# Performance work log

Hardware: AMD Instinct MI355X
Metric: run time of the kernel (lower is better)

## Reference

```python
import jax, jax.numpy as jnp
import numpy as np

HARDLIM_THRESH = 0.2


def setup_inputs() -> dict:
    key = jax.random.key(0)
    k_inp, k_w1, k_b1, k_w2, k_b2 = jax.random.split(key, 5)
    B, D, H, F = 16384, 4096, 2048, 512
    scale1 = 1.0 / np.sqrt(D)
    scale2 = 1.0 / np.sqrt(H)
    return {
        "inp": jax.random.normal(k_inp, (B, D), dtype=jnp.float32),
        "W1": jax.random.normal(k_w1, (H, D), dtype=jnp.float32) * scale1,
        "b1": jax.random.normal(k_b1, (H,), dtype=jnp.float32) * scale1,
        "W2": jax.random.normal(k_w2, (F, H), dtype=jnp.float32) * scale2,
        "b2": jax.random.normal(k_b2, (F,), dtype=jnp.float32) * scale2,
        "k": 8,
    }


def reference(inp, W1, b1, W2, b2, k):
    # Linear -> ReLU -> Linear
    h = jax.nn.relu(inp @ W1.T + b1)            # [B, H]
    logits = h @ W2.T + b2                      # [B, F]
    # 'hard' attention: sigmoid -> keep top-k (zero the rest) -> hardlim(0.2)
    s = jax.nn.sigmoid(logits)
    topk_vals, _ = jax.lax.top_k(s, k)          # [B, k]
    kth = topk_vals[:, -1:]                     # per-row k-th largest value
    gated = jnp.where(s >= kth, s, 0.0)         # GetTopK: zero non-top-k entries
    out = jnp.where(gated > HARDLIM_THRESH, 1.0, 0.0).astype(inp.dtype)
    return out
```

## Files before the change

kernel.cpp:

```cpp
#include <hip/hip_runtime.h>
#include <math.h>
#include <type_traits>


#define BM 128
#define BN 128
#define BK 16
#define BKF 32

#define TAU   1.0e-4f
#define L02F -1.3862943611198906f

typedef __attribute__((ext_vector_type(8))) short bf16x8;
typedef __attribute__((ext_vector_type(4))) float f32x4;

__device__ inline ushort bfhi(float f)   { return (ushort)(__float_as_uint(f) >> 16); }
__device__ inline float  bfhif(float f)  { return __uint_as_float(__float_as_uint(f) & 0xFFFF0000u); }

__global__ __launch_bounds__(256) void split_kernel(
    const float* __restrict__ src, ushort* __restrict__ hi,
    ushort* __restrict__ lo, size_t n4)
{
    size_t i = (size_t)blockIdx.x * 256 + threadIdx.x;
    size_t stride = (size_t)gridDim.x * 256;
    for (; i < n4; i += stride) {
        float4 v = ((const float4*)src)[i];
        ushort4 h, l;
        h.x = bfhi(v.x); l.x = bfhi(v.x - bfhif(v.x));
        h.y = bfhi(v.y); l.y = bfhi(v.y - bfhif(v.y));
        h.z = bfhi(v.z); l.z = bfhi(v.z - bfhif(v.z));
        h.w = bfhi(v.w); l.w = bfhi(v.w - bfhif(v.w));
        ((ushort4*)hi)[i] = h;
        ((ushort4*)lo)[i] = l;
    }
}

template<int A_PRESPLIT, int W_PRESPLIT, int OUT_MODE>
__global__ __launch_bounds__(256) void bgemm_split(
    const float*  __restrict__ A32,
    const ushort* __restrict__ Ahg, const ushort* __restrict__ Alg, int lda,
    const float*  __restrict__ W32,
    const ushort* __restrict__ Whg, const ushort* __restrict__ Wlg, int ldw,
    const float*  __restrict__ bias,
    ushort* __restrict__ Chi, ushort* __restrict__ Clo,
    float*  __restrict__ C32, int N, int K)
{
    __shared__ __align__(16) ushort Ah[BM * BKF];
    __shared__ __align__(16) ushort Al[BM * BKF];
    __shared__ __align__(16) ushort Bh[BN * BKF];
    __shared__ __align__(16) ushort Bl[BN * BKF];

    const int t    = threadIdx.x;
    const int lane = t & 63;
    const int wave = t >> 6;
    const int wr   = wave >> 1;
    const int wc   = wave & 1;
    const int l15  = lane & 15;
    const int l4   = lane >> 4;
    const size_t bm = blockIdx.x;
    const size_t bn = blockIdx.y;

    f32x4 acc[4][4];
    #pragma unroll
    for (int mi = 0; mi < 4; ++mi)
        #pragma unroll
        for (int ni = 0; ni < 4; ++ni)
            acc[mi][ni] = (f32x4){0.f, 0.f, 0.f, 0.f};

    for (int k0 = 0; k0 < K; k0 += BKF) {
        if (A_PRESPLIT) {
            #pragma unroll
            for (int i = 0; i < 2; ++i) {
                int c = t + i * 256;
                int row = c >> 2, q = c & 3;
                size_t g = (bm * BM + row) * (size_t)lda + k0 + q * 8;
                *(uint4*)&Ah[row * BKF + q * 8] = *(const uint4*)(Ahg + g);
                *(uint4*)&Al[row * BKF + q * 8] = *(const uint4*)(Alg + g);
            }
        } else {
            #pragma unroll
            for (int i = 0; i < 4; ++i) {
                int c = t + i * 256;
                int row = c >> 3, q = c & 7;
                float4 v = *(const float4*)(A32 + (bm * BM + row) * (size_t)lda + k0 + q * 4);
                ushort4 h, l;
                h.x = bfhi(v.x); l.x = bfhi(v.x - bfhif(v.x));
                h.y = bfhi(v.y); l.y = bfhi(v.y - bfhif(v.y));
                h.z = bfhi(v.z); l.z = bfhi(v.z - bfhif(v.z));
                h.w = bfhi(v.w); l.w = bfhi(v.w - bfhif(v.w));
                *(ushort4*)&Ah[row * BKF + q * 4] = h;
                *(ushort4*)&Al[row * BKF + q * 4] = l;
            }
        }
        if (W_PRESPLIT) {
            #pragma unroll
            for (int i = 0; i < 2; ++i) {
                int c = t + i * 256;
                int row = c >> 2, q = c & 3;
                size_t g = (bn * BN + row) * (size_t)ldw + k0 + q * 8;
                *(uint4*)&Bh[row * BKF + q * 8] = *(const uint4*)(Whg + g);
                *(uint4*)&Bl[row * BKF + q * 8] = *(const uint4*)(Wlg + g);
            }
        } else {
            #pragma unroll
            for (int i = 0; i < 4; ++i) {
                int c = t + i * 256;
                int row = c >> 3, q = c & 7;
                float4 v = *(const float4*)(W32 + (bn * BN + row) * (size_t)ldw + k0 + q * 4);
                ushort4 h, l;
                h.x = bfhi(v.x); l.x = bfhi(v.x - bfhif(v.x));
                h.y = bfhi(v.y); l.y = bfhi(v.y - bfhif(v.y));
                h.z = bfhi(v.z); l.z = bfhi(v.z - bfhif(v.z));
                h.w = bfhi(v.w); l.w = bfhi(v.w - bfhif(v.w));
                *(ushort4*)&Bh[row * BKF + q * 4] = h;
                *(ushort4*)&Bl[row * BKF + q * 4] = l;
            }
        }
        __syncthreads();

        bf16x8 ah[4], al[4], bh[4], bl[4];
        #pragma unroll
        for (int mi = 0; mi < 4; ++mi) {
            int r = wr * 64 + mi * 16 + l15;
            ah[mi] = *(const bf16x8*)&Ah[r * BKF + l4 * 8];
            al[mi] = *(const bf16x8*)&Al[r * BKF + l4 * 8];
        }
        #pragma unroll
        for (int ni = 0; ni < 4; ++ni) {
            int r = wc * 64 + ni * 16 + l15;
            bh[ni] = *(const bf16x8*)&Bh[r * BKF + l4 * 8];
            bl[ni] = *(const bf16x8*)&Bl[r * BKF + l4 * 8];
        }
        #pragma unroll
        for (int mi = 0; mi < 4; ++mi)
            #pragma unroll
            for (int ni = 0; ni < 4; ++ni) {
                acc[mi][ni] = __builtin_amdgcn_mfma_f32_16x16x32_bf16(ah[mi], bh[ni], acc[mi][ni], 0, 0, 0);
                acc[mi][ni] = __builtin_amdgcn_mfma_f32_16x16x32_bf16(ah[mi], bl[ni], acc[mi][ni], 0, 0, 0);
                acc[mi][ni] = __builtin_amdgcn_mfma_f32_16x16x32_bf16(al[mi], bh[ni], acc[mi][ni], 0, 0, 0);
            }
        __syncthreads();
    }

    #pragma unroll
    for (int ni = 0; ni < 4; ++ni) {
        int col = (int)bn * BN + wc * 64 + ni * 16 + l15;
        float bv = bias[col];
        #pragma unroll
        for (int mi = 0; mi < 4; ++mi) {
            int rowb = (int)bm * BM + wr * 64 + mi * 16 + l4 * 4;
            #pragma unroll
            for (int r = 0; r < 4; ++r) {
                float v = acc[mi][ni][r] + bv;
                size_t idx = (size_t)(rowb + r) * N + col;
                if (OUT_MODE == 0) {
                    v = fmaxf(v, 0.0f);
                    Chi[idx] = bfhi(v);
                    Clo[idx] = bfhi(v - bfhif(v));
                } else {
                    C32[idx] = v;
                }
            }
        }
    }
}

__global__ __launch_bounds__(256) void repair_r1(
    const float* __restrict__ inp,
    const float* __restrict__ W1, const float* __restrict__ b1,
    double* __restrict__ h64,
    const int* __restrict__ risky, const int* __restrict__ cnt, int maxr)
{
    int c = *cnt; if (c > maxr) c = maxr;
    const int by = blockIdx.y;
    if (by * 4 >= c) return;
    __shared__ float Xs[4][4096];
    const int t = threadIdx.x;

    int ridx[4];
    #pragma unroll
    for (int r = 0; r < 4; ++r) {
        int slot = by * 4 + r;
        ridx[r] = risky[slot < c ? slot : (c - 1)];
    }
    #pragma unroll
    for (int i = 0; i < 16; ++i) {
        int lin = t + i * 256;
        int r = lin >> 10, q = lin & 1023;
        *(float4*)&Xs[r][q * 4] = *(const float4*)(inp + (size_t)ridx[r] * 4096 + q * 4);
    }
    __syncthreads();

    const int n0 = blockIdx.x * 512 + t;
    const int n1 = n0 + 256;
    const float* w0 = W1 + (size_t)n0 * 4096;
    const float* w1 = W1 + (size_t)n1 * 4096;
    double acc[2][4] = {};

    for (int k = 0; k < 4096; k += 4) {
        float4 a0 = *(const float4*)(w0 + k);
        float4 a1 = *(const float4*)(w1 + k);
        float xr[4][4];
        #pragma unroll
        for (int r = 0; r < 4; ++r)
            *(float4*)&xr[r][0] = *(const float4*)&Xs[r][k];
        const float* ap0 = &a0.x;
        const float* ap1 = &a1.x;
        #pragma unroll
        for (int j = 0; j < 4; ++j) {
            double wd0 = (double)ap0[j];
            double wd1 = (double)ap1[j];
            #pragma unroll
            for (int r = 0; r < 4; ++r) {
                double xd = (double)xr[r][j];
                acc[0][r] = fma(wd0, xd, acc[0][r]);
                acc[1][r] = fma(wd1, xd, acc[1][r]);
            }
        }
    }

    double bv0 = (double)b1[n0], bv1 = (double)b1[n1];
    #pragma unroll
    for (int r = 0; r < 4; ++r) {
        int slot = by * 4 + r;
        if (slot < c) {
            h64[(size_t)slot * 2048 + n0] = fmax(acc[0][r] + bv0, 0.0);
            h64[(size_t)slot * 2048 + n1] = fmax(acc[1][r] + bv1, 0.0);
        }
    }
}

__global__ __launch_bounds__(256) void repair_r2(
    const double* __restrict__ h64,
    const float* __restrict__ W2, const float* __restrict__ b2,
    double* __restrict__ L64,
    const int* __restrict__ cnt, int maxr)
{
    int c = *cnt; if (c > maxr) c = maxr;
    const int by = blockIdx.y;
    if (by * 4 >= c) return;
    __shared__ double Xs[4][2048];
    const int t = threadIdx.x;

    #pragma unroll
    for (int i = 0; i < 16; ++i) {
        int lin = t + i * 256;
        int r = lin >> 10, q = lin & 1023;
        int slot = by * 4 + r; if (slot >= c) slot = c - 1;
        *(double2*)&Xs[r][q * 2] = *(const double2*)(h64 + (size_t)slot * 2048 + q * 2);
    }
    __syncthreads();

    const int n0 = t;
    const int n1 = t + 256;
    const float* w0 = W2 + (size_t)n0 * 2048;
    const float* w1 = W2 + (size_t)n1 * 2048;
    double acc[2][4] = {};

    for (int k = 0; k < 2048; k += 4) {
        float4 a0 = *(const float4*)(w0 + k);
        float4 a1 = *(const float4*)(w1 + k);
        double xr[4][4];
        #pragma unroll
        for (int r = 0; r < 4; ++r) {
            *(double2*)&xr[r][0] = *(const double2*)&Xs[r][k];
            *(double2*)&xr[r][2] = *(const double2*)&Xs[r][k + 2];
        }
        const float* ap0 = &a0.x;
        const float* ap1 = &a1.x;
        #pragma unroll
        for (int j = 0; j < 4; ++j) {
            double wd0 = (double)ap0[j];
            double wd1 = (double)ap1[j];
            #pragma unroll
            for (int r = 0; r < 4; ++r) {
                acc[0][r] = fma(wd0, xr[r][j], acc[0][r]);
                acc[1][r] = fma(wd1, xr[r][j], acc[1][r]);
            }
        }
    }

    double bv0 = (double)b2[n0], bv1 = (double)b2[n1];
    #pragma unroll
    for (int r = 0; r < 4; ++r) {
        int slot = by * 4 + r;
        if (slot < c) {
            L64[(size_t)slot * 512 + n0] = acc[0][r] + bv0;
            L64[(size_t)slot * 512 + n1] = acc[1][r] + bv1;
        }
    }
}

template<typename TA, int MODE>
__global__ __launch_bounds__(256, 1) void gemm64(
    const TA* __restrict__ A, int lda,
    const float* __restrict__ W, int ldw,
    const float* __restrict__ bias,
    double* __restrict__ out64, int N, int K)
{
    __shared__ double As[BK][BM + 2];
    __shared__ double Bs[BK][BN + 2];
    const int t  = threadIdx.x;
    const int tm = t >> 4;
    const int tn = t & 15;
    const size_t bm = blockIdx.x;
    const size_t bn = blockIdx.y;
    const TA*    Ab = A + bm * BM * (size_t)lda;
    const float* Wb = W + bn * BN * (size_t)ldw;

    double acc[8][8] = {};

    for (int k0 = 0; k0 < K; k0 += BK) {
        #pragma unroll
        for (int i = 0; i < 2; ++i) {
            int f   = t + i * 256;
            int row = f >> 2;
            int kc  = (f & 3) << 2;
            if constexpr (std::is_same<TA, double>::value) {
                double2 v0 = *(const double2*)(Ab + (size_t)row * lda + k0 + kc);
                double2 v1 = *(const double2*)(Ab + (size_t)row * lda + k0 + kc + 2);
                As[kc + 0][row] = v0.x; As[kc + 1][row] = v0.y;
                As[kc + 2][row] = v1.x; As[kc + 3][row] = v1.y;
            } else {
                float4 va = *(const float4*)(Ab + (size_t)row * lda + k0 + kc);
                As[kc + 0][row] = (double)va.x; As[kc + 1][row] = (double)va.y;
                As[kc + 2][row] = (double)va.z; As[kc + 3][row] = (double)va.w;
            }
            float4 vb = *(const float4*)(Wb + (size_t)row * ldw + k0 + kc);
            Bs[kc + 0][row] = (double)vb.x; Bs[kc + 1][row] = (double)vb.y;
            Bs[kc + 2][row] = (double)vb.z; Bs[kc + 3][row] = (double)vb.w;
        }
        __syncthreads();
        #pragma unroll
        for (int k = 0; k < BK; ++k) {
            double a[8], b[8];
            #pragma unroll
            for (int i = 0; i < 4; ++i) {
                *(double2*)&a[i * 2] = *(const double2*)&As[k][tm * 8 + i * 2];
                *(double2*)&b[i * 2] = *(const double2*)&Bs[k][tn * 8 + i * 2];
            }
            #pragma unroll
            for (int i = 0; i < 8; ++i)
                #pragma unroll
                for (int j = 0; j < 8; ++j)
                    acc[i][j] = fma(a[i], b[j], acc[i][j]);
        }
        __syncthreads();
    }

    double bv[8];
    if (MODE != 2) {
        #pragma unroll
        for (int j = 0; j < 8; ++j) bv[j] = (double)bias[bn * BN + tn * 8 + j];
    }

    #pragma unroll
    for (int i = 0; i < 8; ++i) {
        size_t row  = bm * BM + (size_t)tm * 8 + i;
        size_t base = row * (size_t)N + bn * BN + tn * 8;
        #pragma unroll
        for (int j = 0; j < 8; ++j) {
            double v = acc[i][j];
            if (MODE == 0) out64[base + j] = fmax(v + bv[j], 0.0);
            if (MODE == 1) out64[base + j] = v + bv[j];
            if (MODE == 2) out64[base + j] += v;
        }
    }
}

__global__ void init_repair(int* risky, int* cnt, int maxr)
{
    int i = blockIdx.x * 256 + threadIdx.x;
    if (i == 0) *cnt = 0;
    if (i < maxr) risky[i] = 0;
}

__global__ __launch_bounds__(256) void margin_topk32(
    const float* __restrict__ L, float* __restrict__ O, int ncols,
    const int* __restrict__ kp, int* __restrict__ risky, int* __restrict__ cnt,
    int maxr)
{
    const int wave = threadIdx.x >> 6;
    const int lane = threadIdx.x & 63;
    const int k = *kp;
    const size_t row = (size_t)blockIdx.x * 4 + wave;
    const float* Lr = L + row * (size_t)ncols;

    float v[8];
    *(float4*)&v[0] = *(const float4*)(Lr + lane * 8);
    *(float4*)&v[4] = *(const float4*)(Lr + lane * 8 + 4);
    float w[8];
    #pragma unroll
    for (int j = 0; j < 8; ++j) w[j] = v[j];

    float kth = -3.0e38f, minD = 3.0e38f;
    for (int it = 0; it < k; ++it) {
        float mv = w[0]; int mj = 0;
        #pragma unroll
        for (int j = 1; j < 8; ++j)
            if (w[j] > mv) { mv = w[j]; mj = j; }
        int mi = lane * 8 + mj;
        #pragma unroll
        for (int off = 32; off; off >>= 1) {
            float ov = __shfl_xor(mv, off);
            int   oi = __shfl_xor(mi, off);
            if (ov > mv || (ov == mv && oi < mi)) { mv = ov; mi = oi; }
        }
        kth = mv;
        minD = fminf(minD, fabsf(mv - L02F));
        if ((mi >> 3) == lane) w[mi & 7] = -3.0e38f;
    }
    float nv = w[0];
    #pragma unroll
    for (int j = 1; j < 8; ++j) nv = fmaxf(nv, w[j]);
    #pragma unroll
    for (int off = 32; off; off >>= 1) nv = fmaxf(nv, __shfl_xor(nv, off));

    bool risk = ((kth - nv) < 2.0f * TAU) || (minD < TAU);
    if (risk && lane == 0) {
        int p = atomicAdd(cnt, 1);
        if (p < maxr) risky[p] = (int)row;
    }

    float o[8];
    #pragma unroll
    for (int j = 0; j < 8; ++j)
        o[j] = (v[j] >= kth && v[j] > L02F) ? 1.0f : 0.0f;
    float* Op = O + row * (size_t)ncols + lane * 8;
    *(float4*)&Op[0] = *(const float4*)&o[0];
    *(float4*)&Op[4] = *(const float4*)&o[4];
}

__global__ __launch_bounds__(256) void topk64_kernel(
    const double* __restrict__ L, float* __restrict__ O, int ncols,
    const int* __restrict__ kp,
    const int* __restrict__ risky, const int* __restrict__ cnt, int maxr)
{
    const int wave = threadIdx.x >> 6;
    const int lane = threadIdx.x & 63;
    const int k = *kp;
    size_t pos = (size_t)blockIdx.x * 4 + wave;
    size_t row = pos;
    if (cnt) {
        int c = *cnt; if (c > maxr) c = maxr;
        if ((int)pos >= c) return;
        row = (size_t)risky[pos];
    }
    const double* Lr = L + pos * (size_t)ncols;

    double v[8];
    #pragma unroll
    for (int j = 0; j < 8; ++j) {
        double l = Lr[lane * 8 + j];
        v[j] = 1.0 / (1.0 + exp(-l));
    }
    double w[8];
    #pragma unroll
    for (int j = 0; j < 8; ++j) w[j] = v[j];

    double kth = -1.0e300;
    for (int it = 0; it < k; ++it) {
        double mv = w[0]; int mj = 0;
        #pragma unroll
        for (int j = 1; j < 8; ++j)
            if (w[j] > mv) { mv = w[j]; mj = j; }
        int mi = lane * 8 + mj;
        #pragma unroll
        for (int off = 32; off; off >>= 1) {
            double ov = __shfl_xor(mv, off);
            int    oi = __shfl_xor(mi, off);
            if (ov > mv || (ov == mv && oi < mi)) { mv = ov; mi = oi; }
        }
        kth = mv;
        if ((mi >> 3) == lane) w[mi & 7] = -1.0e300;
    }

    float o[8];
    #pragma unroll
    for (int j = 0; j < 8; ++j)
        o[j] = (v[j] >= kth && v[j] > 0.2) ? 1.0f : 0.0f;
    float* Op = O + row * (size_t)ncols + lane * 8;
    *(float4*)&Op[0] = *(const float4*)&o[0];
    *(float4*)&Op[4] = *(const float4*)&o[4];
}

extern "C" void kernel_launch(void* const* d_in, const int* in_sizes, int n_in,
                              void* d_out, int out_size, void* d_ws, size_t ws_size,
                              hipStream_t stream) {
    const float* inp = (const float*)d_in[0];
    const float* W1  = (const float*)d_in[1];
    const float* b1  = (const float*)d_in[2];
    const float* W2  = (const float*)d_in[3];
    const float* b2  = (const float*)d_in[4];
    const int*   kp  = (const int*)d_in[5];

    const int H = in_sizes[2];
    const int F = in_sizes[4];
    const int D = in_sizes[1] / H;
    const int B = in_sizes[0] / D;
    float* out = (float*)d_out;

    const int MAXR = B / 2;
    const size_t szHsplit = (size_t)B * H * 2 * 2;
    const size_t szL32    = (size_t)B * F * 4;
    const size_t szRisky  = (size_t)MAXR * 4 + 256;
    const size_t szW1s    = (size_t)H * D * 2;
    const size_t szW2s    = (size_t)F * H * 2;
    const size_t needC    = szHsplit + szL32 + szRisky;
    const size_t needB    = needC + 2 * szW1s + 2 * szW2s;
    const bool   shapeOK  = (D == 4096 && H == 2048 && F == 512);

    if (shapeOK && ws_size >= needC) {
        ushort* h_hi  = (ushort*)d_ws;
        ushort* h_lo  = h_hi + (size_t)B * H;
        float*  l32   = (float*)((char*)d_ws + szHsplit);
        int*    risky = (int*)((char*)d_ws + szHsplit + szL32);
        int*    cnt   = risky + MAXR;
        double* h64   = (double*)d_ws;
        double* L64   = (double*)((char*)d_ws + szHsplit);

        init_repair<<<(MAXR + 255) / 256, 256, 0, stream>>>(risky, cnt, MAXR);

        if (ws_size >= needB) {
            ushort* w1h = (ushort*)((char*)d_ws + needC);
            ushort* w1l = w1h + (size_t)H * D;
            ushort* w2h = w1l + (size_t)H * D;
            ushort* w2l = w2h + (size_t)F * H;
            split_kernel<<<2048, 256, 0, stream>>>(W1, w1h, w1l, (size_t)H * D / 4);
            split_kernel<<<512, 256, 0, stream>>>(W2, w2h, w2l, (size_t)F * H / 4);
            bgemm_split<0, 1, 0><<<dim3(B / BM, H / BN), 256, 0, stream>>>(
                inp, nullptr, nullptr, D, nullptr, w1h, w1l, D, b1,
                h_hi, h_lo, nullptr, H, D);
            bgemm_split<1, 1, 1><<<dim3(B / BM, F / BN), 256, 0, stream>>>(
                nullptr, h_hi, h_lo, H, nullptr, w2h, w2l, H, b2,
                nullptr, nullptr, l32, F, H);
        } else {
            bgemm_split<0, 0, 0><<<dim3(B / BM, H / BN), 256, 0, stream>>>(
                inp, nullptr, nullptr, D, W1, nullptr, nullptr, D, b1,
                h_hi, h_lo, nullptr, H, D);
            bgemm_split<1, 0, 1><<<dim3(B / BM, F / BN), 256, 0, stream>>>(
                nullptr, h_hi, h_lo, H, W2, nullptr, nullptr, H, b2,
                nullptr, nullptr, l32, F, H);
        }

        margin_topk32<<<B / 4, 256, 0, stream>>>(l32, out, F, kp, risky, cnt, MAXR);
        repair_r1<<<dim3(4, MAXR / 4), 256, 0, stream>>>(
            inp, W1, b1, h64, risky, cnt, MAXR);
        repair_r2<<<dim3(1, MAXR / 4), 256, 0, stream>>>(
            h64, W2, b2, L64, cnt, MAXR);
        topk64_kernel<<<MAXR / 4, 256, 0, stream>>>(L64, out, F, kp, risky, cnt, MAXR);
    } else {
        int Hc = H, Bc = 0;
        for (;;) {
            size_t perRow = (size_t)F * 8 + (size_t)Hc * 8;
            Bc = (int)((ws_size / perRow) / BM) * BM;
            if (Bc >= BM || Hc <= BM) break;
            Hc >>= 1;
        }
        if (Bc < BM) Bc = BM;
        if (Bc > B)  Bc = B;
        double* L   = (double*)d_ws;
        double* h64 = L + (size_t)Bc * F;

        for (int b0 = 0; b0 < B; b0 += Bc) {
            int bc = (B - b0 < Bc) ? (B - b0) : Bc;
            for (int h0 = 0; h0 < H; h0 += Hc) {
                int hc = (H - h0 < Hc) ? (H - h0) : Hc;
                gemm64<float, 0><<<dim3(bc / BM, hc / BN), 256, 0, stream>>>(
                    inp + (size_t)b0 * D, D, W1 + (size_t)h0 * D, D, b1 + h0,
                    h64, hc, D);
                if (h0 == 0)
                    gemm64<double, 1><<<dim3(bc / BM, F / BN), 256, 0, stream>>>(
                        h64, hc, W2 + h0, H, b2, L, F, hc);
                else
                    gemm64<double, 2><<<dim3(bc / BM, F / BN), 256, 0, stream>>>(
                        h64, hc, W2 + h0, H, b2, L, F, hc);
            }
            topk64_kernel<<<bc / 4, 256, 0, stream>>>(
                L, out + (size_t)b0 * F, F, kp, nullptr, nullptr, 0);
        }
    }
}
```

Measured before the change: 1.500 ms.

## Add dedicated 256x128 pipelined first GEMM with direct-to-LDS weight loads

Replaces the generic first-layer split-bf16 GEMM with a specialized 512-thread kernel using 256x128 tiles, a triple-buffered LDS pipeline, and global_load_lds for the pre-split weights. The fp32 input is split into hi/lo inside the kernel, and blocks are remapped with a swizzle for better cache locality. The workspace layout is reworked: logits are written into the output buffer instead of a scratch buffer, and W2 is no longer pre-split, so the second GEMM splits it on the fly. This adds hand-written inline asm wait counts, which risks subtle synchronization bugs, and the kernel is hardcoded to the exact test shape.

```diff
diff --git a/kernel.cpp b/kernel.cpp
--- a/kernel.cpp
+++ b/kernel.cpp
@@ -11,11 +11,18 @@
 #define TAU   1.0e-4f
 #define L02F -1.3862943611198906f
 
-typedef __attribute__((ext_vector_type(8))) short bf16x8;
-typedef __attribute__((ext_vector_type(4))) float f32x4;
+typedef __attribute__((ext_vector_type(8))) short  bf16x8;
+typedef __attribute__((ext_vector_type(8))) ushort u16x8;
+typedef __attribute__((ext_vector_type(4))) float  f32x4;
 
 __device__ inline ushort bfhi(float f)   { return (ushort)(__float_as_uint(f) >> 16); }
 __device__ inline float  bfhif(float f)  { return __uint_as_float(__float_as_uint(f) & 0xFFFF0000u); }
+
+__device__ inline void gload_lds16(const void* g, void* l) {
+    __builtin_amdgcn_global_load_lds(
+        (const __attribute__((address_space(1))) unsigned int*)g,
+        (__attribute__((address_space(3))) unsigned int*)l, 16, 0, 0);
+}
 
 __global__ __launch_bounds__(256) void split_kernel(
     const float* __restrict__ src, ushort* __restrict__ hi,
@@ -33,6 +40,164 @@
         ((ushort4*)hi)[i] = h;
         ((ushort4*)lo)[i] = l;
     }
+}
+
+__global__ __launch_bounds__(512, 2) void bgemm1_8p(
+    const float* __restrict__ inp,
+    const ushort* __restrict__ w1h, const ushort* __restrict__ w1l,
+    const float* __restrict__ b1,
+    ushort* __restrict__ Chi, ushort* __restrict__ Clo)
+{
+    __shared__ ushort lds[73728];
+    const int t    = threadIdx.x;
+    const int lane = t & 63;
+    const int wave = t >> 6;
+    const int wr   = wave >> 1;
+    const int wc   = wave & 1;
+    const int l15  = lane & 15;
+    const int l4   = lane >> 4;
+
+    const int bid = blockIdx.x;
+    const int swz = (bid & 7) * 128 + (bid >> 3);
+    const int bm  = swz & 63;
+    const int bn  = swz >> 6;
+
+    const int ra  = t >> 1;
+    const int kh  = t & 1;
+    const int rb  = t >> 2;
+    const int kqb = (t & 3) ^ (rb & 3);
+
+    const float*  Abase = inp + ((size_t)(bm * 256 + ra)) * 4096 + kh * 16;
+    const ushort* Bsh   = w1h + ((size_t)(bn * 128 + rb)) * 4096 + kqb * 8;
+    const ushort* Bsl   = w1l + ((size_t)(bn * 128 + rb)) * 4096 + kqb * 8;
+
+    f32x4 acc[4][4];
+    #pragma unroll
+    for (int mi = 0; mi < 4; ++mi)
+        #pragma unroll
+        for (int ni = 0; ni < 4; ++ni)
+            acc[mi][ni] = (f32x4){0.f, 0.f, 0.f, 0.f};
+
+    auto a_write = [&](int b, const f32x4 av[4]) {
+        ushort h[16], l[16];
+        #pragma unroll
+        for (int i = 0; i < 4; ++i) {
+            #pragma unroll
+            for (int j = 0; j < 4; ++j) {
+                float x = av[i][j];
+                h[i * 4 + j] = bfhi(x);
+                l[i * 4 + j] = bfhi(x - bfhif(x));
+            }
+        }
+        ushort* A0 = &lds[b * 24576 + ra * 32];
+        #pragma unroll
+        for (int j = 0; j < 2; ++j) {
+            int u = (((2 * kh + j) ^ (ra & 3)) << 3);
+            *(u16x8*)&A0[u]        = *(const u16x8*)&h[j * 8];
+            *(u16x8*)&A0[8192 + u] = *(const u16x8*)&l[j * 8];
+        }
+    };
+    auto w_issue = [&](int b, int kt) {
+        gload_lds16(Bsh + (size_t)kt * 32, &lds[b * 24576 + 16384 + wave * 512]);
+        gload_lds16(Bsl + (size_t)kt * 32, &lds[b * 24576 + 20480 + wave * 512]);
+    };
+    auto a_load_asm = [&](int kt, f32x4 av[4]) {
+        const float* p = Abase + (size_t)kt * 32;
+        asm volatile("global_load_dwordx4 %0, %1, off"           : "=v"(av[0]) : "v"(p));
+        asm volatile("global_load_dwordx4 %0, %1, off offset:16" : "=v"(av[1]) : "v"(p));
+        asm volatile("global_load_dwordx4 %0, %1, off offset:32" : "=v"(av[2]) : "v"(p));
+        asm volatile("global_load_dwordx4 %0, %1, off offset:48" : "=v"(av[3]) : "v"(p));
+    };
+    auto frag_read = [&](int b, bf16x8 ah[4], bf16x8 al[4], bf16x8 bh[4], bf16x8 bl[4]) {
+        const ushort* L0 = &lds[b * 24576];
+        #pragma unroll
+        for (int mi = 0; mi < 4; ++mi) {
+            int row = wr * 64 + mi * 16 + l15;
+            int o = row * 32 + ((l4 ^ (row & 3)) << 3);
+            ah[mi] = *(const bf16x8*)&L0[o];
+            al[mi] = *(const bf16x8*)&L0[8192 + o];
+        }
+        #pragma unroll
+        for (int ni = 0; ni < 4; ++ni) {
+            int row = wc * 64 + ni * 16 + l15;
+            int o = row * 32 + ((l4 ^ (row & 3)) << 3);
+            bh[ni] = *(const bf16x8*)&L0[16384 + o];
+            bl[ni] = *(const bf16x8*)&L0[20480 + o];
+        }
+    };
+    auto do_mfma = [&](bf16x8 ah[4], bf16x8 al[4], bf16x8 bh[4], bf16x8 bl[4]) {
+        __builtin_amdgcn_s_setprio(1);
+        #pragma unroll
+        for (int mi = 0; mi < 4; ++mi)
+            #pragma unroll
+            for (int ni = 0; ni < 4; ++ni) {
+                acc[mi][ni] = __builtin_amdgcn_mfma_f32_16x16x32_bf16(ah[mi], bh[ni], acc[mi][ni], 0, 0, 0);
+                acc[mi][ni] = __builtin_amdgcn_mfma_f32_16x16x32_bf16(ah[mi], bl[ni], acc[mi][ni], 0, 0, 0);
+                acc[mi][ni] = __builtin_amdgcn_mfma_f32_16x16x32_bf16(al[mi], bh[ni], acc[mi][ni], 0, 0, 0);
+            }
+        __builtin_amdgcn_s_setprio(0);
+    };
+    #define BAR_KEEP() asm volatile("s_waitcnt lgkmcnt(0)\n\ts_barrier" ::: "memory")
+
+    {
+        f32x4 av[4];
+        #pragma unroll
+        for (int i = 0; i < 4; ++i) av[i] = *(const f32x4*)(Abase + i * 4);
+        a_write(0, av);
+        w_issue(0, 0);
+        w_issue(1, 1);
+        asm volatile("s_waitcnt vmcnt(0)");
+        BAR_KEEP();
+    }
+
+    bf16x8 ah[4], al[4], bh[4], bl[4];
+    f32x4  av[4];
+    const int nt = 128;
+
+    for (int kt = 0; kt < nt - 2; ++kt) {
+        const int cur = kt % 3, nb1 = (kt + 1) % 3, nb2 = (kt + 2) % 3;
+        frag_read(cur, ah, al, bh, bl);
+        a_load_asm(kt + 1, av);
+        __builtin_amdgcn_sched_barrier(0);
+        w_issue(nb2, kt + 2);
+        __builtin_amdgcn_sched_barrier(0);
+        asm volatile("s_waitcnt vmcnt(2)");
+        asm volatile("" : "+v"(av[0]), "+v"(av[1]), "+v"(av[2]), "+v"(av[3]));
+        a_write(nb1, av);
+        do_mfma(ah, al, bh, bl);
+        BAR_KEEP();
+    }
+    {
+        const int kt = nt - 2;
+        frag_read(kt % 3, ah, al, bh, bl);
+        a_load_asm(kt + 1, av);
+        __builtin_amdgcn_sched_barrier(0);
+        asm volatile("s_waitcnt vmcnt(0)");
+        asm volatile("" : "+v"(av[0]), "+v"(av[1]), "+v"(av[2]), "+v"(av[3]));
+        a_write((kt + 1) % 3, av);
+        do_mfma(ah, al, bh, bl);
+        BAR_KEEP();
+    }
+    frag_read((nt - 1) % 3, ah, al, bh, bl);
+    do_mfma(ah, al, bh, bl);
+
+    #pragma unroll
+    for (int ni = 0; ni < 4; ++ni) {
+        int col = bn * 128 + wc * 64 + ni * 16 + l15;
+        float bv = b1[col];
+        #pragma unroll
+        for (int mi = 0; mi < 4; ++mi) {
+            int rowb = bm * 256 + wr * 64 + mi * 16 + l4 * 4;
+            #pragma unroll
+            for (int r = 0; r < 4; ++r) {
+                float v = fmaxf(acc[mi][ni][r] + bv, 0.0f);
+                size_t idx = (size_t)(rowb + r) * 2048 + col;
+                Chi[idx] = bfhi(v);
+                Clo[idx] = bfhi(v - bfhif(v));
+            }
+        }
+    }
+    #undef BAR_KEEP
 }
 
 template<int A_PRESPLIT, int W_PRESPLIT, int OUT_MODE>
@@ -376,7 +541,7 @@
 }
 
 __global__ __launch_bounds__(256) void margin_topk32(
-    const float* __restrict__ L, float* __restrict__ O, int ncols,
+    const float* L, float* O, int ncols,
     const int* __restrict__ kp, int* __restrict__ risky, int* __restrict__ cnt,
     int maxr)
 {
@@ -500,49 +665,29 @@
     const int B = in_sizes[0] / D;
     float* out = (float*)d_out;
 
-    const int MAXR = B / 2;
-    const size_t szHsplit = (size_t)B * H * 2 * 2;
-    const size_t szL32    = (size_t)B * F * 4;
-    const size_t szRisky  = (size_t)MAXR * 4 + 256;
-    const size_t szW1s    = (size_t)H * D * 2;
-    const size_t szW2s    = (size_t)F * H * 2;
-    const size_t needC    = szHsplit + szL32 + szRisky;
-    const size_t needB    = needC + 2 * szW1s + 2 * szW2s;
-    const bool   shapeOK  = (D == 4096 && H == 2048 && F == 512);
-
-    if (shapeOK && ws_size >= needC) {
+    const int MAXR = 8192;
+    const size_t szHpair = (size_t)B * H * 4;
+    const size_t szW1p   = (size_t)H * D * 4;
+    const size_t needMain = szHpair + szW1p + (size_t)MAXR * 4 + 256;
+    const bool shapeOK = (D == 4096 && H == 2048 && F == 512 && B == 16384);
+
+    if (shapeOK && ws_size >= needMain) {
         ushort* h_hi  = (ushort*)d_ws;
         ushort* h_lo  = h_hi + (size_t)B * H;
-        float*  l32   = (float*)((char*)d_ws + szHsplit);
-        int*    risky = (int*)((char*)d_ws + szHsplit + szL32);
+        ushort* w1h   = (ushort*)((char*)d_ws + szHpair);
+        ushort* w1l   = w1h + (size_t)H * D;
+        int*    risky = (int*)((char*)d_ws + szHpair + szW1p);
         int*    cnt   = risky + MAXR;
         double* h64   = (double*)d_ws;
-        double* L64   = (double*)((char*)d_ws + szHsplit);
+        double* L64   = (double*)((char*)d_ws + szHpair);
+        float*  l32   = out;
 
         init_repair<<<(MAXR + 255) / 256, 256, 0, stream>>>(risky, cnt, MAXR);
-
-        if (ws_size >= needB) {
-            ushort* w1h = (ushort*)((char*)d_ws + needC);
-            ushort* w1l = w1h + (size_t)H * D;
-            ushort* w2h = w1l + (size_t)H * D;
-            ushort* w2l = w2h + (size_t)F * H;
-            split_kernel<<<2048, 256, 0, stream>>>(W1, w1h, w1l, (size_t)H * D / 4);
-            split_kernel<<<512, 256, 0, stream>>>(W2, w2h, w2l, (size_t)F * H / 4);
-            bgemm_split<0, 1, 0><<<dim3(B / BM, H / BN), 256, 0, stream>>>(
-                inp, nullptr, nullptr, D, nullptr, w1h, w1l, D, b1,
-                h_hi, h_lo, nullptr, H, D);
-            bgemm_split<1, 1, 1><<<dim3(B / BM, F / BN), 256, 0, stream>>>(
-                nullptr, h_hi, h_lo, H, nullptr, w2h, w2l, H, b2,
-                nullptr, nullptr, l32, F, H);
-        } else {
-            bgemm_split<0, 0, 0><<<dim3(B / BM, H / BN), 256, 0, stream>>>(
-                inp, nullptr, nullptr, D, W1, nullptr, nullptr, D, b1,
-                h_hi, h_lo, nullptr, H, D);
-            bgemm_split<1, 0, 1><<<dim3(B / BM, F / BN), 256, 0, stream>>>(
-                nullptr, h_hi, h_lo, H, W2, nullptr, nullptr, H, b2,
-                nullptr, nullptr, l32, F, H);
-        }
-
+        split_kernel<<<2048, 256, 0, stream>>>(W1, w1h, w1l, (size_t)H * D / 4);
+        bgemm1_8p<<<1024, 512, 0, stream>>>(inp, w1h, w1l, b1, h_hi, h_lo);
+        bgemm_split<1, 0, 1><<<dim3(B / BM, F / BN), 256, 0, stream>>>(
+            nullptr, h_hi, h_lo, H, W2, nullptr, nullptr, H, b2,
+            nullptr, nullptr, l32, F, H);
         margin_topk32<<<B / 4, 256, 0, stream>>>(l32, out, F, kp, risky, cnt, MAXR);
         repair_r1<<<dim3(4, MAXR / 4), 256, 0, stream>>>(
             inp, W1, b1, h64, risky, cnt, MAXR);
```

Measured after the change: 1.709 ms. 1.14x slower.
